# Optimization experiments

Hardware: AMD Instinct MI355X
Metric: run time of the kernel (lower is better)

## Reference

```python
import jax, jax.numpy as jnp
import numpy as np

EPS = 1e-6

def _phi(x):
    # elu_feature_map: elu(x) + 1 (positive feature map)
    return jax.nn.elu(x) + 1.0

def setup_inputs() -> dict:
    key = jax.random.key(0)
    ks = jax.random.split(key, 6)
    N, L, S, H, E, D = 4, 2048, 2048, 16, 64, 64
    return {
        "queries1": jax.random.normal(ks[0], (N, L, H, E), jnp.float32),
        "keys1": jax.random.normal(ks[1], (N, S, H, E), jnp.float32),
        "values1": jax.random.normal(ks[2], (N, S, H, D), jnp.float32),
        "queries2": jax.random.normal(ks[3], (N, L, H, E), jnp.float32),
        "keys2": jax.random.normal(ks[4], (N, S, H, E), jnp.float32),
        "values2": jax.random.normal(ks[5], (N, S, H, D), jnp.float32),
        "key_lengths1": jnp.ones((N, S), jnp.float32),
        "key_lengths2": jnp.ones((N, S), jnp.float32),
    }

def _linear_cross(Q, K_other, V_other):
    # Q: (N,L,H,E) featurized queries; K_other: (N,S,H,E) featurized+masked keys
    # KV: (N,H,D,E) ; 'nshd,nshm->nhmd'
    KV = jnp.einsum('nshd,nshm->nhmd', K_other, V_other)
    Ksum = K_other.sum(axis=1)                      # (N,H,E)
    Z = 1.0 / (jnp.einsum('nlhd,nhd->nlh', Q, Ksum) + EPS)
    # 'nlhd,nhmd,nlh->nlhm'
    return jnp.einsum('nlhd,nhmd->nlhm', Q, KV) * Z[..., None]

def reference(queries1, keys1, values1, queries2, keys2, values2,
              key_lengths1, key_lengths2):
    Q1 = _phi(queries1)
    K1 = _phi(keys1) * key_lengths1[:, :, None, None]
    Q2 = _phi(queries2)
    K2 = _phi(keys2) * key_lengths2[:, :, None, None]
    V1 = _linear_cross(Q1, K2, values2)  # stream1 queries attend to stream2 keys/values
    V2 = _linear_cross(Q2, K1, values1)  # stream2 queries attend to stream1 keys/values
    return (V1, V2)
```

## Files before the change

### kernel.cpp

```cpp
#include <hip/hip_runtime.h>

#define NB 4
#define LL 2048
#define SS 2048
#define HH 16
#define EE 64
#define DD 64

#define NHEAD (2*NB*HH)
#define NCHUNK 8
#define KVP ((size_t)NHEAD*NCHUNK*4096)
#define WSFLOATS (KVP + (size_t)NHEAD*NCHUNK*64)

typedef short short8 __attribute__((ext_vector_type(8)));
typedef float floatx4 __attribute__((ext_vector_type(4)));

__device__ inline float phi(float x) { return x > 0.f ? x + 1.f : __expf(x); }

__device__ inline unsigned int f2bf(float f) {
    unsigned int x = __float_as_uint(f);
    return (x + 0x7FFFu + ((x >> 16) & 1u)) >> 16;
}
__device__ inline void split_pack(float a, float b, unsigned int &hp, unsigned int &lp) {
    const unsigned int ha = f2bf(a), hb = f2bf(b);
    const float ra = a - __uint_as_float(ha << 16);
    const float rb = b - __uint_as_float(hb << 16);
    hp = (ha & 0xFFFFu) | (hb << 16);
    lp = (f2bf(ra) & 0xFFFFu) | (f2bf(rb) << 16);
}

__device__ inline int swz(int row, int col) {
    return ((((col >> 3) ^ ((row >> 2) ^ row)) & 7) << 3) | (col & 7);
}

__global__ __launch_bounds__(256) void kv_kernel(
    const float* __restrict__ k1, const float* __restrict__ v1,
    const float* __restrict__ k2, const float* __restrict__ v2,
    const float* __restrict__ kl1, const float* __restrict__ kl2,
    float* __restrict__ ws)
{
    const int b = blockIdx.x;
    const int chunk = b & 7;
    const int h = (b >> 3) & 15;
    const int n = (b >> 7) & 3;
    const int st = (b >> 9) & 1;
    const float* K  = st ? k1 : k2;
    const float* V  = st ? v1 : v2;
    const float* KL = st ? kl1 : kl2;

    __shared__ __align__(16) unsigned short KtH[64][64];
    __shared__ __align__(16) unsigned short KtL[64][64];
    __shared__ __align__(16) unsigned short VtH[64][64];
    __shared__ __align__(16) unsigned short VtL[64][64];

    const int t = threadIdx.x;
    const int lane = t & 63;
    const int w = t >> 6;
    const int d4 = t & 15;
    const int sp = t >> 4;
    const int c = lane & 15;
    const int q = lane >> 4;

    float ksum[4] = {0.f, 0.f, 0.f, 0.f};
    floatx4 acc[4];
#pragma unroll
    for (int i = 0; i < 4; i++) acc[i] = (floatx4){0.f, 0.f, 0.f, 0.f};

    float4 cur[8]; float curl[4];
    {
        const int sbase = chunk * 256;
#pragma unroll
        for (int i = 0; i < 2; ++i) {
            const int sl = 2 * sp + 32 * i;
            const size_t off = ((size_t)((size_t)n * SS + sbase + sl) * HH + h) * EE + 4 * d4;
            cur[4 * i + 0] = *(const float4*)&K[off];
            cur[4 * i + 1] = *(const float4*)&K[off + HH * EE];
            cur[4 * i + 2] = *(const float4*)&V[off];
            cur[4 * i + 3] = *(const float4*)&V[off + HH * EE];
            curl[2 * i + 0] = KL[(size_t)n * SS + sbase + sl];
            curl[2 * i + 1] = KL[(size_t)n * SS + sbase + sl + 1];
        }
    }

    for (int g = 0; g < 4; ++g) {
        float4 nxt[8]; float nxtl[4];
        if (g < 3) {
            const int sbase = chunk * 256 + (g + 1) * 64;
#pragma unroll
            for (int i = 0; i < 2; ++i) {
                const int sl = 2 * sp + 32 * i;
                const size_t off = ((size_t)((size_t)n * SS + sbase + sl) * HH + h) * EE + 4 * d4;
                nxt[4 * i + 0] = *(const float4*)&K[off];
                nxt[4 * i + 1] = *(const float4*)&K[off + HH * EE];
                nxt[4 * i + 2] = *(const float4*)&V[off];
                nxt[4 * i + 3] = *(const float4*)&V[off + HH * EE];
                nxtl[2 * i + 0] = KL[(size_t)n * SS + sbase + sl];
                nxtl[2 * i + 1] = KL[(size_t)n * SS + sbase + sl + 1];
            }
        }
        if (g) __syncthreads();
#pragma unroll
        for (int i = 0; i < 2; ++i) {
            const int sl = 2 * sp + 32 * i;
            const float4 ka = cur[4 * i + 0], kb = cur[4 * i + 1];
            const float4 va = cur[4 * i + 2], vb = cur[4 * i + 3];
            const float l0 = curl[2 * i + 0], l1 = curl[2 * i + 1];
            const float a0 = phi(ka.x) * l0, a1 = phi(ka.y) * l0;
            const float a2 = phi(ka.z) * l0, a3 = phi(ka.w) * l0;
            const float b0 = phi(kb.x) * l1, b1 = phi(kb.y) * l1;
            const float b2 = phi(kb.z) * l1, b3 = phi(kb.w) * l1;
            ksum[0] += a0 + b0; ksum[1] += a1 + b1;
            ksum[2] += a2 + b2; ksum[3] += a3 + b3;
            unsigned int hp, lp;
            const int r0 = 4 * d4;
            const int s0 = swz(r0 + 0, sl), s1 = swz(r0 + 1, sl);
            const int s2 = swz(r0 + 2, sl), s3 = swz(r0 + 3, sl);
            split_pack(a0, b0, hp, lp);
            *(unsigned int*)&KtH[r0 + 0][s0] = hp; *(unsigned int*)&KtL[r0 + 0][s0] = lp;
            split_pack(a1, b1, hp, lp);
            *(unsigned int*)&KtH[r0 + 1][s1] = hp; *(unsigned int*)&KtL[r0 + 1][s1] = lp;
            split_pack(a2, b2, hp, lp);
            *(unsigned int*)&KtH[r0 + 2][s2] = hp; *(unsigned int*)&KtL[r0 + 2][s2] = lp;
            split_pack(a3, b3, hp, lp);
            *(unsigned int*)&KtH[r0 + 3][s3] = hp; *(unsigned int*)&KtL[r0 + 3][s3] = lp;
            split_pack(va.x, vb.x, hp, lp);
            *(unsigned int*)&VtH[r0 + 0][s0] = hp; *(unsigned int*)&VtL[r0 + 0][s0] = lp;
            split_pack(va.y, vb.y, hp, lp);
            *(unsigned int*)&VtH[r0 + 1][s1] = hp; *(unsigned int*)&VtL[r0 + 1][s1] = lp;
            split_pack(va.z, vb.z, hp, lp);
            *(unsigned int*)&VtH[r0 + 2][s2] = hp; *(unsigned int*)&VtL[r0 + 2][s2] = lp;
            split_pack(va.w, vb.w, hp, lp);
            *(unsigned int*)&VtH[r0 + 3][s3] = hp; *(unsigned int*)&VtL[r0 + 3][s3] = lp;
        }
        __syncthreads();
        const int ra = 16 * w + c;
#pragma unroll
        for (int ks = 0; ks < 2; ++ks) {
            const int ca = swz(ra, 32 * ks + 8 * q);
            const short8 aH = *(const short8*)&VtH[ra][ca];
            const short8 aL = *(const short8*)&VtL[ra][ca];
#pragma unroll
            for (int dt = 0; dt < 4; ++dt) {
                const int rb = 16 * dt + c;
                const int cb = swz(rb, 32 * ks + 8 * q);
                const short8 bH = *(const short8*)&KtH[rb][cb];
                const short8 bL = *(const short8*)&KtL[rb][cb];
                acc[dt] = __builtin_amdgcn_mfma_f32_16x16x32_bf16(aH, bH, acc[dt], 0, 0, 0);
                acc[dt] = __builtin_amdgcn_mfma_f32_16x16x32_bf16(aH, bL, acc[dt], 0, 0, 0);
                acc[dt] = __builtin_amdgcn_mfma_f32_16x16x32_bf16(aL, bH, acc[dt], 0, 0, 0);
            }
        }
        if (g < 3) {
#pragma unroll
            for (int i = 0; i < 8; ++i) cur[i] = nxt[i];
#pragma unroll
            for (int i = 0; i < 4; ++i) curl[i] = nxtl[i];
        }
    }

    const int head = (st * NB + n) * HH + h;
    const size_t kvbase = ((size_t)head * NCHUNK + chunk) * 4096;
#pragma unroll
    for (int dt = 0; dt < 4; ++dt)
#pragma unroll
        for (int r = 0; r < 4; ++r)
            ws[kvbase + (size_t)(16 * w + 4 * q + r) * 64 + 16 * dt + c] = acc[dt][r];

    float (*scr)[64] = (float(*)[64])VtL;
    __syncthreads();
    scr[sp][4 * d4 + 0] = ksum[0];
    scr[sp][4 * d4 + 1] = ksum[1];
    scr[sp][4 * d4 + 2] = ksum[2];
    scr[sp][4 * d4 + 3] = ksum[3];
    __syncthreads();
    if (t < 64) {
        float s = 0.f;
#pragma unroll
        for (int i = 0; i < 16; ++i) s += scr[i][t];
        ws[KVP + ((size_t)head * NCHUNK + chunk) * 64 + t] = s;
    }
}

static __device__ __forceinline__ float lt_body(
    const float4 qa0, const float4 qb0, const float4 qa1, const float4 qb1,
    const float* Ksp,
    const unsigned short (*BH)[72], const unsigned short (*BL)[72],
    const int c, const int q, floatx4* acc)
{
    float z = 0.f;
#pragma unroll
    for (int ks = 0; ks < 2; ++ks) {
        const float4 qa = ks ? qa1 : qa0;
        const float4 qb = ks ? qb1 : qb0;
        const int co = 32 * ks + 8 * q;
        const float p[8] = {phi(qa.x), phi(qa.y), phi(qa.z), phi(qa.w),
                            phi(qb.x), phi(qb.y), phi(qb.z), phi(qb.w)};
        z += p[0] * Ksp[co + 0] + p[1] * Ksp[co + 1]
           + p[2] * Ksp[co + 2] + p[3] * Ksp[co + 3]
           + p[4] * Ksp[co + 4] + p[5] * Ksp[co + 5]
           + p[6] * Ksp[co + 6] + p[7] * Ksp[co + 7];
        short8 aH, aL;
#pragma unroll
        for (int j = 0; j < 8; ++j) {
            const unsigned int hb = f2bf(p[j]);
            aH[j] = (short)hb;
            aL[j] = (short)f2bf(p[j] - __uint_as_float(hb << 16));
        }
#pragma unroll
        for (int mt = 0; mt < 4; ++mt) {
            const short8 bH = *(const short8*)&BH[16 * mt + c][co];
            const short8 bL = *(const short8*)&BL[16 * mt + c][co];
            acc[mt] = __builtin_amdgcn_mfma_f32_16x16x32_bf16(aH, bH, acc[mt], 0, 0, 0);
            acc[mt] = __builtin_amdgcn_mfma_f32_16x16x32_bf16(aH, bL, acc[mt], 0, 0, 0);
            acc[mt] = __builtin_amdgcn_mfma_f32_16x16x32_bf16(aL, bH, acc[mt], 0, 0, 0);
        }
    }
    return z;
}

__global__ __launch_bounds__(256) void out_kernel(
    const float* __restrict__ q1, const float* __restrict__ q2,
    const float* __restrict__ ws, float* __restrict__ out)
{
    const int b = blockIdx.x;
    const int lc = b & 15;
    const int h = (b >> 4) & 15;
    const int n = (b >> 8) & 3;
    const int st = (b >> 10) & 1;
    const float* Q = st ? q2 : q1;
    float* O = out + (size_t)st * ((size_t)NB * LL * HH * DD);

    __shared__ __align__(16) unsigned short BtH[64][72];
    __shared__ __align__(16) unsigned short BtL[64][72];
    __shared__ float Ks[64];

    const int t = threadIdx.x;
    const int lane = t & 63;
    const int w = t >> 6;
    const int c = lane & 15;
    const int q = lane >> 4;
    const int head = (st * NB + n) * HH + h;
    const size_t kvb8 = (size_t)head * NCHUNK * 4096;
    const int lbase = lc * 128;

    const float* qr0 = &Q[((size_t)((size_t)n * LL + lbase + 32 * w + c) * HH + h) * EE];
    const int d0q = 8 * q;
    const float4 p00 = *(const float4*)&qr0[d0q];
    const float4 p01 = *(const float4*)&qr0[d0q + 4];
    const float4 p02 = *(const float4*)&qr0[d0q + 32];
    const float4 p03 = *(const float4*)&qr0[d0q + 36];

    {
        const int m = t >> 2;
        const int dbase = (t & 3) * 16;
#pragma unroll
        for (int i = 0; i < 4; ++i) {
            const int d0 = dbase + 4 * i;
            const size_t eo = (size_t)m * 64 + d0;
            float4 kv = *(const float4*)&ws[kvb8 + eo];
#pragma unroll
            for (int ch = 1; ch < NCHUNK; ++ch) {
                const float4 p = *(const float4*)&ws[kvb8 + (size_t)ch * 4096 + eo];
                kv.x += p.x; kv.y += p.y; kv.z += p.z; kv.w += p.w;
            }
            unsigned int hp, lp;
            split_pack(kv.x, kv.y, hp, lp);
            *(unsigned int*)&BtH[m][d0]     = hp; *(unsigned int*)&BtL[m][d0]     = lp;
            split_pack(kv.z, kv.w, hp, lp);
            *(unsigned int*)&BtH[m][d0 + 2] = hp; *(unsigned int*)&BtL[m][d0 + 2] = lp;
        }
    }
    if (t < 64) {
        float s = 0.f;
#pragma unroll
        for (int ch = 0; ch < NCHUNK; ++ch)
            s += ws[KVP + ((size_t)head * NCHUNK + ch) * 64 + t];
        Ks[t] = s;
    }
    __syncthreads();

    floatx4 acc[8];
#pragma unroll
    for (int i = 0; i < 8; ++i) acc[i] = (floatx4){0.f, 0.f, 0.f, 0.f};

    float z0 = lt_body(p00, p01, p02, p03, Ks, BtH, BtL, c, q, acc);

    const float* qr1 = qr0 + (size_t)16 * HH * EE;
    const float4 p10 = *(const float4*)&qr1[d0q];
    const float4 p11 = *(const float4*)&qr1[d0q + 4];
    const float4 p12 = *(const float4*)&qr1[d0q + 32];
    const float4 p13 = *(const float4*)&qr1[d0q + 36];
    float z1 = lt_body(p10, p11, p12, p13, Ks, BtH, BtL, c, q, acc + 4);

    z0 += __shfl_xor(z0, 16); z0 += __shfl_xor(z0, 32);
    z1 += __shfl_xor(z1, 16); z1 += __shfl_xor(z1, 32);
    const float zi0 = 1.f / (z0 + 1e-6f);
    const float zi1 = 1.f / (z1 + 1e-6f);

#pragma unroll
    for (int lt = 0; lt < 2; ++lt) {
        const float zi = lt ? zi1 : zi0;
#pragma unroll
        for (int r = 0; r < 4; ++r) {
            const float zz = __shfl(zi, 4 * q + r);
            const int ll = 32 * w + 16 * lt + 4 * q + r;
            const size_t ro = ((size_t)((size_t)n * LL + lbase + ll) * HH + h) * DD;
#pragma unroll
            for (int mt = 0; mt < 4; ++mt)
                O[ro + 16 * mt + c] = acc[4 * lt + mt][r] * zz;
        }
    }
}

extern "C" void kernel_launch(void* const* d_in, const int* in_sizes, int n_in,
                              void* d_out, int out_size, void* d_ws, size_t ws_size,
                              hipStream_t stream) {
    const float* q1  = (const float*)d_in[0];
    const float* k1  = (const float*)d_in[1];
    const float* v1  = (const float*)d_in[2];
    const float* q2  = (const float*)d_in[3];
    const float* k2  = (const float*)d_in[4];
    const float* v2  = (const float*)d_in[5];
    const float* kl1 = (const float*)d_in[6];
    const float* kl2 = (const float*)d_in[7];
    float* ws = (float*)d_ws;
    float* out = (float*)d_out;

    kv_kernel<<<dim3(1024), dim3(256), 0, stream>>>(k1, v1, k2, v2, kl1, kl2, ws);
    out_kernel<<<dim3(2048), dim3(256), 0, stream>>>(q1, q2, ws, out);
}
```

Baseline: 276.4 us.

## Hoist per-head KV chunk reduction and bf16 split into separate reduce kernel

```diff
diff --git a/kernel.cpp b/kernel.cpp
--- a/kernel.cpp
+++ b/kernel.cpp
@@ -181,10 +181,54 @@
     }
 }
 
+__global__ __launch_bounds__(256) void reduce_kernel(float* __restrict__ ws)
+{
+    const int head = blockIdx.x;
+    const int t = threadIdx.x;
+    const size_t base = (size_t)head * (NCHUNK * 4096);
+    const int m = t >> 2;
+    const int dbase = (t & 3) * 16;
+
+    float4 kv[4];
+#pragma unroll
+    for (int i = 0; i < 4; ++i) {
+        const int d0 = dbase + 4 * i;
+        const size_t eo = (size_t)m * 64 + d0;
+        float4 s = *(const float4*)&ws[base + eo];
+#pragma unroll
+        for (int ch = 1; ch < NCHUNK; ++ch) {
+            const float4 p = *(const float4*)&ws[base + (size_t)ch * 4096 + eo];
+            s.x += p.x; s.y += p.y; s.z += p.z; s.w += p.w;
+        }
+        kv[i] = s;
+    }
+    float ks = 0.f;
+    if (t < 64) {
+#pragma unroll
+        for (int ch = 0; ch < NCHUNK; ++ch)
+            ks += ws[KVP + ((size_t)head * NCHUNK + ch) * 64 + t];
+    }
+    __syncthreads();
+
+    const int fm = ((m >> 2) ^ m) & 7;
+    unsigned int* W = (unsigned int*)&ws[base];
+#pragma unroll
+    for (int i = 0; i < 4; ++i) {
+        const int d0 = dbase + 4 * i;
+        const int bp = ((((d0 >> 3) ^ fm) & 7) << 2) + ((d0 & 4) >> 1);
+        unsigned int hp, lp;
+        split_pack(kv[i].x, kv[i].y, hp, lp);
+        W[m * 32 + bp]     = hp;  W[2048 + m * 32 + bp]     = lp;
+        split_pack(kv[i].z, kv[i].w, hp, lp);
+        W[m * 32 + bp + 1] = hp;  W[2048 + m * 32 + bp + 1] = lp;
+    }
+    if (t < 64) ws[KVP + (size_t)head * NCHUNK * 64 + t] = ks;
+}
+
 static __device__ __forceinline__ float lt_body(
     const float4 qa0, const float4 qb0, const float4 qa1, const float4 qb1,
     const float* Ksp,
-    const unsigned short (*BH)[72], const unsigned short (*BL)[72],
+    const unsigned short (*BH)[64], const unsigned short (*BL)[64],
     const int c, const int q, floatx4* acc)
 {
     float z = 0.f;
@@ -208,8 +252,10 @@
         }
 #pragma unroll
         for (int mt = 0; mt < 4; ++mt) {
-            const short8 bH = *(const short8*)&BH[16 * mt + c][co];
-            const short8 bL = *(const short8*)&BL[16 * mt + c][co];
+            const int rb = 16 * mt + c;
+            const int cb = swz(rb, co);
+            const short8 bH = *(const short8*)&BH[rb][cb];
+            const short8 bL = *(const short8*)&BL[rb][cb];
             acc[mt] = __builtin_amdgcn_mfma_f32_16x16x32_bf16(aH, bH, acc[mt], 0, 0, 0);
             acc[mt] = __builtin_amdgcn_mfma_f32_16x16x32_bf16(aH, bL, acc[mt], 0, 0, 0);
             acc[mt] = __builtin_amdgcn_mfma_f32_16x16x32_bf16(aL, bH, acc[mt], 0, 0, 0);
@@ -230,8 +276,8 @@
     const float* Q = st ? q2 : q1;
     float* O = out + (size_t)st * ((size_t)NB * LL * HH * DD);
 
-    __shared__ __align__(16) unsigned short BtH[64][72];
-    __shared__ __align__(16) unsigned short BtL[64][72];
+    __shared__ __align__(16) unsigned short BtH[64][64];
+    __shared__ __align__(16) unsigned short BtL[64][64];
     __shared__ float Ks[64];
 
     const int t = threadIdx.x;
@@ -240,7 +286,6 @@
     const int c = lane & 15;
     const int q = lane >> 4;
     const int head = (st * NB + n) * HH + h;
-    const size_t kvb8 = (size_t)head * NCHUNK * 4096;
     const int lbase = lc * 128;
 
     const float* qr0 = &Q[((size_t)((size_t)n * LL + lbase + 32 * w + c) * HH + h) * EE];
@@ -249,47 +294,29 @@
     const float4 p01 = *(const float4*)&qr0[d0q + 4];
     const float4 p02 = *(const float4*)&qr0[d0q + 32];
     const float4 p03 = *(const float4*)&qr0[d0q + 36];
-
-    {
-        const int m = t >> 2;
-        const int dbase = (t & 3) * 16;
-#pragma unroll
-        for (int i = 0; i < 4; ++i) {
-            const int d0 = dbase + 4 * i;
-            const size_t eo = (size_t)m * 64 + d0;
-            float4 kv = *(const float4*)&ws[kvb8 + eo];
-#pragma unroll
-            for (int ch = 1; ch < NCHUNK; ++ch) {
-                const float4 p = *(const float4*)&ws[kvb8 + (size_t)ch * 4096 + eo];
-                kv.x += p.x; kv.y += p.y; kv.z += p.z; kv.w += p.w;
-            }
-            unsigned int hp, lp;
-            split_pack(kv.x, kv.y, hp, lp);
-            *(unsigned int*)&BtH[m][d0]     = hp; *(unsigned int*)&BtL[m][d0]     = lp;
-            split_pack(kv.z, kv.w, hp, lp);
-            *(unsigned int*)&BtH[m][d0 + 2] = hp; *(unsigned int*)&BtL[m][d0 + 2] = lp;
-        }
-    }
-    if (t < 64) {
-        float s = 0.f;
-#pragma unroll
-        for (int ch = 0; ch < NCHUNK; ++ch)
-            s += ws[KVP + ((size_t)head * NCHUNK + ch) * 64 + t];
-        Ks[t] = s;
-    }
-    __syncthreads();
-
-    floatx4 acc[8];
-#pragma unroll
-    for (int i = 0; i < 8; ++i) acc[i] = (floatx4){0.f, 0.f, 0.f, 0.f};
-
-    float z0 = lt_body(p00, p01, p02, p03, Ks, BtH, BtL, c, q, acc);
-
     const float* qr1 = qr0 + (size_t)16 * HH * EE;
     const float4 p10 = *(const float4*)&qr1[d0q];
     const float4 p11 = *(const float4*)&qr1[d0q + 4];
     const float4 p12 = *(const float4*)&qr1[d0q + 32];
     const float4 p13 = *(const float4*)&qr1[d0q + 36];
+
+    {
+        const uint4* src = (const uint4*)(ws + (size_t)head * (NCHUNK * 4096));
+        uint4* dstH = (uint4*)&BtH[0][0];
+        uint4* dstL = (uint4*)&BtL[0][0];
+        dstH[t]       = src[t];
+        dstH[t + 256] = src[t + 256];
+        dstL[t]       = src[512 + t];
+        dstL[t + 256] = src[768 + t];
+    }
+    if (t < 64) Ks[t] = ws[KVP + (size_t)head * NCHUNK * 64 + t];
+    __syncthreads();
+
+    floatx4 acc[8];
+#pragma unroll
+    for (int i = 0; i < 8; ++i) acc[i] = (floatx4){0.f, 0.f, 0.f, 0.f};
+
+    float z0 = lt_body(p00, p01, p02, p03, Ks, BtH, BtL, c, q, acc);
     float z1 = lt_body(p10, p11, p12, p13, Ks, BtH, BtL, c, q, acc + 4);
 
     z0 += __shfl_xor(z0, 16); z0 += __shfl_xor(z0, 32);
@@ -327,5 +354,6 @@
     float* out = (float*)d_out;
 
     kv_kernel<<<dim3(1024), dim3(256), 0, stream>>>(k1, v1, k2, v2, kl1, kl2, ws);
+    reduce_kernel<<<dim3(128), dim3(256), 0, stream>>>(ws);
     out_kernel<<<dim3(2048), dim3(256), 0, stream>>>(q1, q2, ws, out);
 }
```

Result: faster. 240.8 us (-12.9%).
